# Optimization experiments

Hardware: AMD Instinct MI355X
Metric: run time of the kernel (lower is better)

Reference implementation:

```python
import jax, jax.numpy as jnp
import numpy as np

PAD_IDX = 1
B, L, E, H = 2, 256, 512, 8
D = E // H
SCALE = D ** -0.5


def setup_inputs() -> dict:
    key = jax.random.key(0)
    ks = jax.random.split(key, 10)
    std = 0.02
    return {
        "queries": jax.random.normal(ks[0], (B, L, E), jnp.float32),
        "keys": jax.random.normal(ks[1], (B, L, E), jnp.float32),
        "values": jax.random.normal(ks[2], (B, L, E), jnp.float32),
        "relation": jax.random.normal(ks[3], (B, L, L, E), jnp.float32),
        "adj_mask": jax.random.randint(ks[4], (B, L, L), 0, 2, jnp.int32),
        "Wq": jax.random.normal(ks[5], (E, E), jnp.float32) * std,
        "bq": jnp.zeros((E,), jnp.float32),
        "Wk": jax.random.normal(ks[6], (E, E), jnp.float32) * std,
        "bk": jnp.zeros((E,), jnp.float32),
        "Wv": jax.random.normal(ks[7], (E, E), jnp.float32) * std,
        "bv": jnp.zeros((E,), jnp.float32),
        "Wr": jax.random.normal(ks[8], (2 * E, E), jnp.float32) * std,
        "Wo": jax.random.normal(ks[9], (E, E), jnp.float32) * std,
        "bo": jnp.zeros((E,), jnp.float32),
    }


def reference(queries, keys, values, relation, adj_mask,
              Wq, bq, Wk, bk, Wv, bv, Wr, Wo, bo):
    b, t, _ = queries.shape
    s = keys.shape[1]
    # input projections (torch Linear: y = x @ W.T + b)
    q = ((queries @ Wq.T + bq) * SCALE).reshape(b, t, H, D)
    k = (keys @ Wk.T + bk).reshape(b, s, H, D)
    v = (values @ Wv.T + bv).reshape(b, s, H, D)
    # relation projection -> relation queries/keys, [b, t, s, H, D] then transpose(1,2)
    rel = relation @ Wr.T                              # [b, t, s, 2E]
    rq, rk = jnp.split(rel, 2, axis=-1)
    rq = rq.reshape(b, t, s, H, D).transpose(0, 2, 1, 3, 4)  # [b, s, t, H, D]
    rk = rk.reshape(b, t, s, H, D).transpose(0, 2, 1, 3, 4)
    # broadcasted relation bias (requires t == s, as in the original)
    qe = q[:, :, None] + rq                            # [b, t, s, H, D]
    ke = k[:, None] + rk                               # [b, t, s, H, D]
    attn = jnp.einsum('bijhn,bijhn->bijh', qe, ke)     # [b, t, s, H]
    pad = (adj_mask == PAD_IDX)[..., None]             # [b, t, s, 1]
    attn = jnp.where(pad, -jnp.inf, attn)
    attn_weights = jax.nn.softmax(attn, axis=2)
    out = jnp.einsum('bijh,bjhn->bihn', attn_weights, v).reshape(b, t, E)
    out = out @ Wo.T + bo
    return out, attn_weights
```

## Files before the change

### kernel.cpp

```cpp
#include <hip/hip_runtime.h>

typedef unsigned int uint32;
typedef unsigned short ushort16;
typedef __attribute__((ext_vector_type(8))) short bf16x8;
typedef __attribute__((ext_vector_type(4))) float f32x4;


__device__ __forceinline__ uint32 bf_rne(uint32 u) {
  return (u + 0x7fffu + ((u >> 16) & 1u)) >> 16;
}

__global__ void cvt_wr_kernel(const float* __restrict__ Wr, ushort16* __restrict__ WrBf) {
  int idx = blockIdx.x * 256 + threadIdx.x;
  const uint4* src = (const uint4*)Wr;
  uint4 x = src[idx];
  uint2 o;
  o.x = bf_rne(x.x) | (bf_rne(x.y) << 16);
  o.y = bf_rne(x.z) | (bf_rne(x.w) << 16);
  ((uint2*)WrBf)[idx] = o;
}

__global__ __launch_bounds__(256) void proj_kernel(
    const float* __restrict__ X0, const float* __restrict__ W0, const float* __restrict__ b0, float* __restrict__ Y0,
    const float* __restrict__ X1, const float* __restrict__ W1, const float* __restrict__ b1, float* __restrict__ Y1,
    const float* __restrict__ X2, const float* __restrict__ W2, const float* __restrict__ b2, float* __restrict__ Y2,
    float scale0) {
  int z = blockIdx.z;
  const float* X = (z == 0) ? X0 : (z == 1) ? X1 : X2;
  const float* W = (z == 0) ? W0 : (z == 1) ? W1 : W2;
  const float* bias = (z == 0) ? b0 : (z == 1) ? b1 : b2;
  float* Y = (z == 0) ? Y0 : (z == 1) ? Y1 : Y2;
  float scale = (z == 0) ? scale0 : 1.0f;

  __shared__ float Xs[16][68];
  __shared__ float Ws[16][68];

  int tid = threadIdx.x;
  int tx = tid & 15, ty = tid >> 4;
  int m0 = blockIdx.x * 64, n0 = blockIdx.y * 64;

  float acc[4][4] = {};

  for (int k0 = 0; k0 < 512; k0 += 16) {
#pragma unroll
    for (int u = 0; u < 4; ++u) {
      int idx = tid + u * 256;
      int ml = idx >> 4, kl = idx & 15;
      Xs[kl][ml] = X[(size_t)(m0 + ml) * 512 + k0 + kl];
      Ws[kl][ml] = W[(size_t)(n0 + ml) * 512 + k0 + kl];
    }
    __syncthreads();
#pragma unroll
    for (int kk = 0; kk < 16; ++kk) {
      float4 a = *(const float4*)&Xs[kk][ty * 4];
      float4 w = *(const float4*)&Ws[kk][tx * 4];
      float av[4] = {a.x, a.y, a.z, a.w};
      float wv[4] = {w.x, w.y, w.z, w.w};
#pragma unroll
      for (int i = 0; i < 4; ++i)
#pragma unroll
        for (int jj = 0; jj < 4; ++jj)
          acc[i][jj] += av[i] * wv[jj];
    }
    __syncthreads();
  }
#pragma unroll
  for (int i = 0; i < 4; ++i) {
    int m = m0 + ty * 4 + i;
#pragma unroll
    for (int jj = 0; jj < 4; ++jj) {
      int n = n0 + tx * 4 + jj;
      Y[(size_t)m * 512 + n] = (acc[i][jj] + bias[n]) * scale;
    }
  }
}

__global__ __launch_bounds__(256, 3) void rel_score_kernel(
    const float* __restrict__ rel,
    const ushort16* __restrict__ wrbf,
    const float* __restrict__ qws,
    const float* __restrict__ kws,
    float* __restrict__ attn)
{
  __shared__ ushort16 As[64 * 64];
  __shared__ ushort16 Bs[256 * 64];
  __shared__ float scores[4][64];

  const int tid = threadIdx.x;
  const int lane = tid & 63;
  const int wv = tid >> 6;
  const int blk = blockIdx.x;
  const int hp = blk & 3;
  const int mt = blk >> 2;
  const int b = mt >> 10;
  const int j = (mt >> 2) & 255;
  const int i0 = (mt & 3) << 6;
  const int h0 = hp << 1;

  const float* Abase = rel + (size_t)mt * (64 * 512);

  int gOff[8];
#pragma unroll
  for (int v = 0; v < 8; ++v) {
    int r_local = wv * 64 + v * 8 + (lane >> 3);
    int hl = r_local >> 7;
    int nn = r_local & 127;
    int g = nn >> 4, t = nn & 15;
    int wr_row = (g & 1) * 512 + (h0 + hl) * 64 + (g >> 1) * 16 + t;
    gOff[v] = wr_row * 512 + (lane & 7) * 8;
  }

  const int arow0 = tid >> 3;
  const int ak8 = (tid & 7) * 8;

  f32x4 acc[4][4];
#pragma unroll
  for (int a = 0; a < 4; ++a)
#pragma unroll
    for (int c = 0; c < 4; ++c)
      acc[a][c] = (f32x4){0.f, 0.f, 0.f, 0.f};

  const int t15 = lane & 15;
  const int kq = (lane >> 4) * 8;

  for (int k0 = 0; k0 < 512; k0 += 64) {
#pragma unroll
    for (int u = 0; u < 2; ++u) {
      int row = arow0 + u * 32;
      const uint4* src = (const uint4*)(Abase + (size_t)row * 512 + k0 + ak8);
      uint4 x = src[0];
      uint4 y = src[1];
      uint4 o;
      o.x = (x.y & 0xffff0000u) | (x.x >> 16);
      o.y = (x.w & 0xffff0000u) | (x.z >> 16);
      o.z = (y.y & 0xffff0000u) | (y.x >> 16);
      o.w = (y.w & 0xffff0000u) | (y.z >> 16);
      *(uint4*)&As[row * 64 + ak8] = o;
    }
#pragma unroll
    for (int v = 0; v < 8; ++v) {
      __builtin_amdgcn_global_load_lds(
          (const __attribute__((address_space(1))) void*)(wrbf + gOff[v] + k0),
          (__attribute__((address_space(3))) void*)&Bs[wv * 4096 + v * 512],
          16, 0, 0);
    }
    __syncthreads();
#pragma unroll
    for (int kh = 0; kh < 2; ++kh) {
      int kk = kh * 32 + kq;
      bf16x8 af[4], bfr[4];
#pragma unroll
      for (int fr = 0; fr < 4; ++fr)
        af[fr] = *(const bf16x8*)&As[(fr * 16 + t15) * 64 + kk];
#pragma unroll
      for (int fc = 0; fc < 4; ++fc)
        bfr[fc] = *(const bf16x8*)&Bs[(wv * 64 + fc * 16 + t15) * 64 + kk];
#pragma unroll
      for (int fr = 0; fr < 4; ++fr)
#pragma unroll
        for (int fc = 0; fc < 4; ++fc)
          acc[fr][fc] = __builtin_amdgcn_mfma_f32_16x16x32_bf16(
              af[fr], bfr[fc], acc[fr][fc], 0, 0, 0);
    }
    __syncthreads();
  }

  const int hthis = h0 + (wv >> 1);
  const int dbase = (wv & 1) * 32;
  const float* qbase = qws + ((size_t)(b * 256 + i0)) * 512 + hthis * 64;
  const float* krow = kws + ((size_t)(b * 256 + j)) * 512 + hthis * 64;
  const int rgrp = lane >> 4;
#pragma unroll
  for (int fr = 0; fr < 4; ++fr) {
#pragma unroll
    for (int r = 0; r < 4; ++r) {
      int m = fr * 16 + rgrp * 4 + r;
      float s = 0.f;
#pragma unroll
      for (int p = 0; p < 2; ++p) {
        int d = dbase + p * 16 + t15;
        float qv = qbase[(size_t)m * 512 + d];
        float kv = krow[d];
        s += (qv + acc[fr][p * 2][r]) * (kv + acc[fr][p * 2 + 1][r]);
      }
      s += __shfl_xor(s, 1);
      s += __shfl_xor(s, 2);
      s += __shfl_xor(s, 4);
      s += __shfl_xor(s, 8);
      if (t15 == 0) scores[wv][m] = s;
    }
  }
  __syncthreads();
  if (tid < 128) {
    int hl = tid >> 6, m = tid & 63;
    float sc = scores[hl * 2][m] + scores[hl * 2 + 1][m];
    attn[(((size_t)(b * 256 + i0 + m)) * 256 + j) * 8 + (h0 + hl)] = sc;
  }
}

__global__ __launch_bounds__(256) void softmax_kernel(float* __restrict__ attn,
                                                      const int* __restrict__ adj) {
  __shared__ float sl[2048];
  __shared__ int msk[256];
  int bi = blockIdx.x;
  float* base = attn + (size_t)bi * 2048;
  const int* abase = adj + (size_t)bi * 256;
  int tid = threadIdx.x;
#pragma unroll
  for (int u = 0; u < 8; ++u) sl[tid + u * 256] = base[tid + u * 256];
  msk[tid] = abase[tid];
  __syncthreads();
  int h = tid >> 5, l5 = tid & 31;
  float mx = -INFINITY;
#pragma unroll
  for (int u = 0; u < 8; ++u) {
    int jj = l5 + u * 32;
    if (msk[jj] != 1) mx = fmaxf(mx, sl[jj * 8 + h]);
  }
#pragma unroll
  for (int off = 16; off >= 1; off >>= 1) mx = fmaxf(mx, __shfl_xor(mx, off));
  float ev[8];
  float sum = 0.f;
#pragma unroll
  for (int u = 0; u < 8; ++u) {
    int jj = l5 + u * 32;
    float e = (msk[jj] != 1) ? __expf(sl[jj * 8 + h] - mx) : 0.f;
    ev[u] = e;
    sum += e;
  }
#pragma unroll
  for (int off = 16; off >= 1; off >>= 1) sum += __shfl_xor(sum, off);
  float inv = (sum > 0.f) ? (1.f / sum) : 0.f;
#pragma unroll
  for (int u = 0; u < 8; ++u) {
    int jj = l5 + u * 32;
    sl[jj * 8 + h] = ev[u] * inv;
  }
  __syncthreads();
#pragma unroll
  for (int u = 0; u < 8; ++u) base[tid + u * 256] = sl[tid + u * 256];
}

__global__ __launch_bounds__(256) void av_kernel(const float* __restrict__ attn,
                                                 const float* __restrict__ vws,
                                                 float* __restrict__ o1) {
  int bi = blockIdx.x;
  int b = bi >> 8;
  int tid = threadIdx.x;
  const float* wbase = attn + (size_t)bi * 2048;
  const float* vbase = vws + (size_t)b * (256 * 512);
  int e0 = tid, e1 = tid + 256;
  int h0 = e0 >> 6, h1 = e1 >> 6;
  float a0 = 0.f, a1 = 0.f;
  for (int jj = 0; jj < 256; ++jj) {
    float w0 = wbase[jj * 8 + h0];
    float w1 = wbase[jj * 8 + h1];
    const float* vr = vbase + (size_t)jj * 512;
    a0 += w0 * vr[e0];
    a1 += w1 * vr[e1];
  }
  float* orow = o1 + (size_t)bi * 512;
  orow[e0] = a0;
  orow[e1] = a1;
}

extern "C" void kernel_launch(void* const* d_in, const int* in_sizes, int n_in,
                              void* d_out, int out_size, void* d_ws, size_t ws_size,
                              hipStream_t stream) {
  const float* queries = (const float*)d_in[0];
  const float* keys    = (const float*)d_in[1];
  const float* values  = (const float*)d_in[2];
  const float* relation = (const float*)d_in[3];
  const int*   adj     = (const int*)d_in[4];
  const float* Wq = (const float*)d_in[5];
  const float* bq = (const float*)d_in[6];
  const float* Wk = (const float*)d_in[7];
  const float* bk = (const float*)d_in[8];
  const float* Wv = (const float*)d_in[9];
  const float* bv = (const float*)d_in[10];
  const float* Wr = (const float*)d_in[11];
  const float* Wo = (const float*)d_in[12];
  const float* bo = (const float*)d_in[13];

  float* out  = (float*)d_out;
  float* attn = out + 262144;

  float* ws  = (float*)d_ws;
  float* qws = ws;
  float* kws = ws + 262144;
  float* vws = ws + 524288;
  float* o1  = ws + 786432;
  ushort16* wrbf = (ushort16*)(ws + 1048576);

  cvt_wr_kernel<<<dim3(512), dim3(256), 0, stream>>>(Wr, wrbf);

  proj_kernel<<<dim3(8, 8, 3), dim3(256), 0, stream>>>(
      queries, Wq, bq, qws,
      keys,    Wk, bk, kws,
      values,  Wv, bv, vws,
      0.125f);

  rel_score_kernel<<<dim3(8192), dim3(256), 0, stream>>>(relation, wrbf, qws, kws, attn);

  softmax_kernel<<<dim3(512), dim3(256), 0, stream>>>(attn, adj);

  av_kernel<<<dim3(512), dim3(256), 0, stream>>>(attn, vws, o1);

  proj_kernel<<<dim3(8, 8, 1), dim3(256), 0, stream>>>(
      o1, Wo, bo, out,
      nullptr, nullptr, nullptr, nullptr,
      nullptr, nullptr, nullptr, nullptr,
      1.0f);
}
```

Before: 713.7 us.

## Load Wr fragments directly to registers, pad A tile, fuse softmax with AV

The relation-score GEMM now reads bf16 Wr fragments straight from global memory into registers rather than staging them in a 32KB shared tile with global_load_lds. This shrinks LDS use, allowing more resident blocks. The A tile row stride is padded from 64 to 72 elements to cut LDS bank conflicts. Softmax and the attention-times-V step are merged into one kernel that reads the normalized weights from shared memory, dropping a launch and a global reread, at the cost of exposed global latency on the B loads.

```diff
diff --git a/kernel.cpp b/kernel.cpp
--- a/kernel.cpp
+++ b/kernel.cpp
@@ -1,7 +1,6 @@
 #include <hip/hip_runtime.h>
 
 typedef unsigned int uint32;
-typedef unsigned short ushort16;
 typedef __attribute__((ext_vector_type(8))) short bf16x8;
 typedef __attribute__((ext_vector_type(4))) float f32x4;
 
@@ -10,7 +9,7 @@
   return (u + 0x7fffu + ((u >> 16) & 1u)) >> 16;
 }
 
-__global__ void cvt_wr_kernel(const float* __restrict__ Wr, ushort16* __restrict__ WrBf) {
+__global__ void cvt_wr_kernel(const float* __restrict__ Wr, unsigned short* __restrict__ WrBf) {
   int idx = blockIdx.x * 256 + threadIdx.x;
   const uint4* src = (const uint4*)Wr;
   uint4 x = src[idx];
@@ -77,13 +76,12 @@
 
 __global__ __launch_bounds__(256, 3) void rel_score_kernel(
     const float* __restrict__ rel,
-    const ushort16* __restrict__ wrbf,
+    const unsigned short* __restrict__ wrbf,
     const float* __restrict__ qws,
     const float* __restrict__ kws,
     float* __restrict__ attn)
 {
-  __shared__ ushort16 As[64 * 64];
-  __shared__ ushort16 Bs[256 * 64];
+  __shared__ unsigned short As[64 * 72];
   __shared__ float scores[4][64];
 
   const int tid = threadIdx.x;
@@ -99,15 +97,15 @@
 
   const float* Abase = rel + (size_t)mt * (64 * 512);
 
-  int gOff[8];
-#pragma unroll
-  for (int v = 0; v < 8; ++v) {
-    int r_local = wv * 64 + v * 8 + (lane >> 3);
-    int hl = r_local >> 7;
-    int nn = r_local & 127;
-    int g = nn >> 4, t = nn & 15;
-    int wr_row = (g & 1) * 512 + (h0 + hl) * 64 + (g >> 1) * 16 + t;
-    gOff[v] = wr_row * 512 + (lane & 7) * 8;
+  const int t15 = lane & 15;
+  const int kq = (lane >> 4) * 8;
+
+  const unsigned short* bptr[4];
+#pragma unroll
+  for (int fc = 0; fc < 4; ++fc) {
+    int g = (wv & 1) * 4 + fc;
+    int wr_row = (g & 1) * 512 + (h0 + (wv >> 1)) * 64 + (g >> 1) * 16 + t15;
+    bptr[fc] = wrbf + (size_t)wr_row * 512 + kq;
   }
 
   const int arow0 = tid >> 3;
@@ -120,10 +118,13 @@
     for (int c = 0; c < 4; ++c)
       acc[a][c] = (f32x4){0.f, 0.f, 0.f, 0.f};
 
-  const int t15 = lane & 15;
-  const int kq = (lane >> 4) * 8;
-
   for (int k0 = 0; k0 < 512; k0 += 64) {
+    bf16x8 bfr[2][4];
+#pragma unroll
+    for (int kh = 0; kh < 2; ++kh)
+#pragma unroll
+      for (int fc = 0; fc < 4; ++fc)
+        bfr[kh][fc] = *(const bf16x8*)(bptr[fc] + k0 + kh * 32);
 #pragma unroll
     for (int u = 0; u < 2; ++u) {
       int row = arow0 + u * 32;
@@ -135,32 +136,22 @@
       o.y = (x.w & 0xffff0000u) | (x.z >> 16);
       o.z = (y.y & 0xffff0000u) | (y.x >> 16);
       o.w = (y.w & 0xffff0000u) | (y.z >> 16);
-      *(uint4*)&As[row * 64 + ak8] = o;
-    }
-#pragma unroll
-    for (int v = 0; v < 8; ++v) {
-      __builtin_amdgcn_global_load_lds(
-          (const __attribute__((address_space(1))) void*)(wrbf + gOff[v] + k0),
-          (__attribute__((address_space(3))) void*)&Bs[wv * 4096 + v * 512],
-          16, 0, 0);
+      *(uint4*)&As[row * 72 + ak8] = o;
     }
     __syncthreads();
 #pragma unroll
     for (int kh = 0; kh < 2; ++kh) {
       int kk = kh * 32 + kq;
-      bf16x8 af[4], bfr[4];
+      bf16x8 af[4];
 #pragma unroll
       for (int fr = 0; fr < 4; ++fr)
-        af[fr] = *(const bf16x8*)&As[(fr * 16 + t15) * 64 + kk];
-#pragma unroll
-      for (int fc = 0; fc < 4; ++fc)
-        bfr[fc] = *(const bf16x8*)&Bs[(wv * 64 + fc * 16 + t15) * 64 + kk];
+        af[fr] = *(const bf16x8*)&As[(fr * 16 + t15) * 72 + kk];
 #pragma unroll
       for (int fr = 0; fr < 4; ++fr)
 #pragma unroll
         for (int fc = 0; fc < 4; ++fc)
           acc[fr][fc] = __builtin_amdgcn_mfma_f32_16x16x32_bf16(
-              af[fr], bfr[fc], acc[fr][fc], 0, 0, 0);
+              af[fr], bfr[kh][fc], acc[fr][fc], 0, 0, 0);
     }
     __syncthreads();
   }
@@ -198,11 +189,13 @@
   }
 }
 
-__global__ __launch_bounds__(256) void softmax_kernel(float* __restrict__ attn,
-                                                      const int* __restrict__ adj) {
+__global__ __launch_bounds__(256) void softmax_av_kernel(
+    float* __restrict__ attn, const int* __restrict__ adj,
+    const float* __restrict__ vws, float* __restrict__ o1) {
   __shared__ float sl[2048];
   __shared__ int msk[256];
   int bi = blockIdx.x;
+  int b = bi >> 8;
   float* base = attn + (size_t)bi * 2048;
   const int* abase = adj + (size_t)bi * 256;
   int tid = threadIdx.x;
@@ -239,22 +232,13 @@
   __syncthreads();
 #pragma unroll
   for (int u = 0; u < 8; ++u) base[tid + u * 256] = sl[tid + u * 256];
-}
-
-__global__ __launch_bounds__(256) void av_kernel(const float* __restrict__ attn,
-                                                 const float* __restrict__ vws,
-                                                 float* __restrict__ o1) {
-  int bi = blockIdx.x;
-  int b = bi >> 8;
-  int tid = threadIdx.x;
-  const float* wbase = attn + (size_t)bi * 2048;
   const float* vbase = vws + (size_t)b * (256 * 512);
   int e0 = tid, e1 = tid + 256;
   int h0 = e0 >> 6, h1 = e1 >> 6;
   float a0 = 0.f, a1 = 0.f;
   for (int jj = 0; jj < 256; ++jj) {
-    float w0 = wbase[jj * 8 + h0];
-    float w1 = wbase[jj * 8 + h1];
+    float w0 = sl[jj * 8 + h0];
+    float w1 = sl[jj * 8 + h1];
     const float* vr = vbase + (size_t)jj * 512;
     a0 += w0 * vr[e0];
     a1 += w1 * vr[e1];
@@ -290,7 +274,7 @@
   float* kws = ws + 262144;
   float* vws = ws + 524288;
   float* o1  = ws + 786432;
-  ushort16* wrbf = (ushort16*)(ws + 1048576);
+  unsigned short* wrbf = (unsigned short*)(ws + 1048576);
 
   cvt_wr_kernel<<<dim3(512), dim3(256), 0, stream>>>(Wr, wrbf);
 
@@ -302,9 +286,7 @@
 
   rel_score_kernel<<<dim3(8192), dim3(256), 0, stream>>>(relation, wrbf, qws, kws, attn);
 
-  softmax_kernel<<<dim3(512), dim3(256), 0, stream>>>(attn, adj);
-
-  av_kernel<<<dim3(512), dim3(256), 0, stream>>>(attn, vws, o1);
+  softmax_av_kernel<<<dim3(512), dim3(256), 0, stream>>>(attn, adj, vws, o1);
 
   proj_kernel<<<dim3(8, 8, 1), dim3(256), 0, stream>>>(
       o1, Wo, bo, out,
```

Measured after the change: 730.9 us. 2.4% more time.
